# Optimization experiments

Hardware: AMD Instinct MI355X
Metric: run time of the kernel (lower is better)

## Reference

```python
import jax, jax.numpy as jnp
import numpy as np

SCALE = 10.0
KB = 1.0  # kernel_bandwidth

B, D, P, M, K = 128, 128, 4, 100000, 10


def _sqdist(a, b):
    # a: [..., N, D], b: [..., M, D] -> squared euclidean [..., N, M]
    a2 = jnp.sum(a * a, axis=-1)[..., :, None]
    b2 = jnp.sum(b * b, axis=-1)[..., None, :]
    ab = jnp.einsum('...nd,...md->...nm', a, b)
    return jnp.maximum(a2 + b2 - 2.0 * ab, 0.0)


def setup_inputs() -> dict:
    key = jax.random.key(0)
    k1, k2, k3, k4, k5, k6, k7 = jax.random.split(key, 7)
    return {
        'global_img_feat': jax.random.normal(k1, (B, D), jnp.float32),
        'global_text_feat': jax.random.normal(k2, (B, D), jnp.float32),
        'local_img_feats': jax.random.normal(k3, (P, B, D), jnp.float32),
        'centers': jax.random.normal(k4, (P, M, D), jnp.float32),
        'cross_indices': jax.random.randint(k5, (B, K), 0, M, jnp.int64),
        'position': jax.random.randint(k6, (B,), 0, M, jnp.int64),
        'memory_vid': jax.random.randint(k7, (M,), 0, 1000, jnp.int64),
    }


def reference(global_img_feat, global_text_feat, local_img_feats, centers,
              cross_indices, position, memory_vid):
    b = global_img_feat.shape[0]
    # ---- global MMD alignment (text branch detached) ----
    img = global_img_feat / jnp.linalg.norm(global_img_feat, axis=1, keepdims=True)
    txt_d = jax.lax.stop_gradient(global_text_feat)
    txt = txt_d / jnp.linalg.norm(txt_d, axis=1, keepdims=True)
    inv2kb2 = 1.0 / (2.0 * KB * KB)
    k_xx = jnp.exp(-_sqdist(img, img) * inv2kb2)
    k_yy = jnp.exp(-_sqdist(txt, txt) * inv2kb2)
    k_xy = jnp.exp(-_sqdist(img, txt) * inv2kb2)
    off = ~jnp.eye(b, dtype=bool)
    denom = b * (b - 1)
    mmd = (jnp.sum(jnp.where(off, k_xx, 0.0)) / denom
           + jnp.sum(jnp.where(off, k_yy, 0.0)) / denom
           - 2.0 * jnp.mean(k_xy))
    # ---- local part contrastive loss (vectorized over P parts) ----
    m = centers.shape[1]
    pos_feat = centers[:, cross_indices]                       # [P,B,K,D]
    f2 = jnp.sum(local_img_feats ** 2, axis=-1)                # [P,B]
    p2 = jnp.sum(pos_feat ** 2, axis=-1)                       # [P,B,K]
    fp = jnp.einsum('pbd,pbkd->pbk', local_img_feats, pos_feat)
    pos_dist = jnp.sqrt(jnp.maximum(f2[..., None] + p2 - 2.0 * fp, 0.0))  # [P,B,K]
    neg_dist = jnp.sqrt(_sqdist(local_img_feats, centers))     # [P,B,M]
    # negative mask over memory slots (int indices are constants)
    neg_mask = jnp.ones((m,), bool).at[cross_indices.reshape(-1)].set(False)
    neg_mask = neg_mask.at[position].set(False)
    x = jnp.log(jnp.sum(jnp.exp(-SCALE * pos_dist), axis=-1))  # [P,B]
    y = jnp.log(jnp.sum(jnp.exp(-SCALE * neg_dist) * neg_mask[None, None, :], axis=-1))
    l = jnp.sum(-x + y, axis=1) / local_img_feats.shape[1]     # [P]
    l = jnp.where(jnp.isnan(l), 0.0, l)
    local_loss = jnp.sum(l) / local_img_feats.shape[0]
    total = local_loss + 1.0 * mmd
    pos_vid = memory_vid[cross_indices]                        # [B,K]
    return total, local_loss, mmd, pos_vid
```

## Files before the change

kernel.cpp:

```cpp
#include <hip/hip_runtime.h>
#include <math.h>

#define B_ 128
#define D_ 128
#define P_ 4
#define M_ 100000
#define K_ 10
#define SCALE_ 10.0f
#define TPP 1563
#define NEG_BLOCKS 256
#define MMD_BLOCKS 128
#define POS_BLOCKS 128
#define D2_CUT 120.0f

typedef short bf16x8 __attribute__((ext_vector_type(8)));
typedef float floatx4 __attribute__((ext_vector_type(4)));

__device__ inline unsigned pack_bf16_trunc(unsigned f0, unsigned f1) {
    return __builtin_amdgcn_perm(f1, f0, 0x07060302u);
}

template <int CTRL>
__device__ inline float dpp_add(float v) {
    int x = __builtin_amdgcn_update_dpp(0, __builtin_bit_cast(int, v), CTRL, 0xF, 0xF, true);
    return v + __builtin_bit_cast(float, x);
}
__device__ inline float row16Sum(float v) {
    v = dpp_add<0xB1>(v);
    v = dpp_add<0x4E>(v);
    v = dpp_add<0x141>(v);
    v = dpp_add<0x140>(v);
    return v;
}
__device__ inline float waveSum64(float v) {
    v = row16Sum(v);
    v += __shfl_xor(v, 16, 64);
    v += __shfl_xor(v, 32, 64);
    return v;
}
__device__ inline float waveReduceSumOld(float v) {
    #pragma unroll
    for (int off = 32; off > 0; off >>= 1) v += __shfl_xor(v, off, 64);
    return v;
}
__device__ inline float blockReduce128(float v, float* sh2) {
    v = waveSum64(v);
    int wid = threadIdx.x >> 6;
    if ((threadIdx.x & 63) == 0) sh2[wid] = v;
    __syncthreads();
    float r = sh2[0] + sh2[1];
    __syncthreads();
    return r;
}

__global__ __launch_bounds__(128) void k_prep(const float* __restrict__ img,
                                              const float* __restrict__ txt,
                                              const float* __restrict__ local,
                                              float* imgT, float* txtT,
                                              float* a2i, float* a2t,
                                              float* f2w, float* s_neg,
                                              bf16x8* __restrict__ Apk) {
    __shared__ float sh2[2];
    int bid = blockIdx.x, t = threadIdx.x;
    if (bid < 256) {
        int row = bid & 127, which = bid >> 7;
        if (bid < 4) s_neg[bid * 128 + t] = 0.f;
        const float* src = which ? txt : img;
        float* dstT = which ? txtT : imgT;
        float* a2 = which ? a2t : a2i;
        float v = src[row * D_ + t];
        float s = blockReduce128(v * v, sh2);
        float n = v / sqrtf(s);
        dstT[t * 128 + row] = n;
        float s2 = blockReduce128(n * n, sh2);
        if (t == 0) a2[row] = s2;
    } else if (bid < 768) {
        int r = bid - 256;
        float v = local[(size_t)r * D_ + t];
        float s = blockReduce128(v * v, sh2);
        if (t == 0) f2w[r] = s;
    } else {
        int g = (bid - 768) * 128 + t;
        int p = g >> 11, f = g & 2047;
        int fl = f & 63, bt = (f >> 6) & 7, kc = f >> 9;
        int row = bt * 16 + (fl & 15);
        int col = kc * 32 + ((fl >> 4) & 3) * 8;
        const float* lp = local + (size_t)p * B_ * D_ + row * D_ + col;
        const uint4 u0 = *(const uint4*)lp;
        const uint4 u1 = *(const uint4*)(lp + 4);
        union { bf16x8 v; unsigned u[4]; } fr;
        fr.u[0] = pack_bf16_trunc(u0.x, u0.y);
        fr.u[1] = pack_bf16_trunc(u0.z, u0.w);
        fr.u[2] = pack_bf16_trunc(u1.x, u1.y);
        fr.u[3] = pack_bf16_trunc(u1.z, u1.w);
        Apk[g] = fr.v;
    }
}

__global__ __launch_bounds__(256, 2) void k_main(const float* __restrict__ local,
                                                 const float* __restrict__ centers,
                                                 const float* __restrict__ imgT,
                                                 const float* __restrict__ txtT,
                                                 const float* __restrict__ a2i,
                                                 const float* __restrict__ a2t,
                                                 const int* __restrict__ ci,
                                                 const int* __restrict__ posi,
                                                 const int* __restrict__ mvid,
                                                 const float* __restrict__ f2w,
                                                 const bf16x8* __restrict__ Apk,
                                                 float* __restrict__ s_neg,
                                                 float* __restrict__ s_pos,
                                                 double* __restrict__ mmd_part,
                                                 float* __restrict__ out) {
    union Smem {
        struct {
            bf16x8 A_lds[2048];
            float Bt[3][8192];
            float sred[512];
            float f2l[128];
        } n;
        struct {
            float ri[128], rt[128];
            float sh2[2];
        } m;
    };
    __shared__ Smem sm;
    const int bid = blockIdx.x;
    const int t = threadIdx.x;
    const int w = t >> 6;
    const int l = t & 63;

    if (bid < NEG_BLOCKS) {
        const int p = bid >> 6;
        const int g = bid & 63;
        const int nt = (g < 27) ? 25 : 24;
        const int n16 = l & 15;
        const int q = l >> 4;

        if (t < 128) sm.n.f2l[t] = f2w[p * 128 + t];

        const bf16x8* Ap = Apk + (p << 11);
        #pragma unroll
        for (int s8 = 0; s8 < 8; s8++) {
            int fb = w * 64 + 256 * s8;
            __builtin_amdgcn_global_load_lds(
                (const __attribute__((address_space(1))) void*)(Ap + fb + l),
                (__attribute__((address_space(3))) void*)(&sm.n.A_lds[fb]),
                16, 0, 0);
        }

        unsigned soff[8];
        #pragma unroll
        for (int j = 0; j < 8; j++) {
            unsigned d = (unsigned)(w * 8 + j) * 1024u + (unsigned)l * 16u;
            unsigned s = 2u * ((d >> 11) & 3u) + ((d >> 8) & 1u);
            unsigned e = d ^ (s << 4);
            unsigned u = e >> 5, hf = (e >> 4) & 1u;
            soff[j] = (u & 63u) * 512u + (u >> 8) * 128u + ((u >> 6) & 3u) * 32u + hf * 16u;
        }

        const char* cbp = (const char*)(centers + (size_t)p * M_ * D_);
        char* BtBase = (char*)&sm.n.Bt[0][0];

        auto DMA_TILE = [&](int m0, int buf) {
            char* dst = BtBase + buf * 32768 + w * 8192;
            if (m0 + 64 <= M_) {
                const char* srcb = cbp + (size_t)m0 * 512;
                #pragma unroll
                for (int j = 0; j < 8; j++) {
                    __builtin_amdgcn_global_load_lds(
                        (const __attribute__((address_space(1))) void*)(srcb + soff[j]),
                        (__attribute__((address_space(3))) void*)(dst + j * 1024),
                        16, 0, 0);
                }
            } else {
                #pragma unroll
                for (int j = 0; j < 8; j++) {
                    unsigned d = (unsigned)(w * 8 + j) * 1024u + (unsigned)l * 16u;
                    unsigned s = 2u * ((d >> 11) & 3u) + ((d >> 8) & 1u);
                    unsigned e = d ^ (s << 4);
                    unsigned u = e >> 5, hf = (e >> 4) & 1u;
                    int row = m0 + (int)(u & 63u);
                    if (row >= M_) row = M_ - 1;
                    size_t off = (size_t)row * 512 + (u >> 8) * 128 + ((u >> 6) & 3u) * 32 + hf * 16;
                    __builtin_amdgcn_global_load_lds(
                        (const __attribute__((address_space(1))) void*)(cbp + off),
                        (__attribute__((address_space(3))) void*)(dst + j * 1024),
                        16, 0, 0);
                }
            }
        };

        float sacc[8][4];
        #pragma unroll
        for (int bt = 0; bt < 8; bt++)
            #pragma unroll
            for (int r = 0; r < 4; r++) sacc[bt][r] = 0.f;

        int m0 = g * 64;
        DMA_TILE(m0, 0);
        if (nt > 1) DMA_TILE(m0 + 4096, 1);
        int bcur = 0;

        for (int i = 0; i < nt; i++) {
            if (i < nt - 1) asm volatile("s_waitcnt vmcnt(8)" ::: "memory");
            else           asm volatile("s_waitcnt vmcnt(0)" ::: "memory");
            __builtin_amdgcn_s_barrier();

            if (i + 2 < nt) {
                int b2 = bcur + 2; if (b2 >= 3) b2 -= 3;
                DMA_TILE(m0 + 8192, b2);
            }

            const char* bufc = (const char*)(BtBase + bcur * 32768);
            float c2 = 0.f;
            bf16x8 bfr[4];
            #pragma unroll
            for (int kc = 0; kc < 4; kc++) {
                unsigned u = (unsigned)((kc * 4 + q) * 64 + (w * 16 + n16));
                unsigned sb = 2u * (unsigned)q + (unsigned)((n16 >> 3) & 1);
                unsigned a0 = (u * 32u) ^ (sb << 4);
                union { floatx4 f; uint4 ui; } h0, h1;
                h0.f = *(const floatx4*)(bufc + a0);
                h1.f = *(const floatx4*)(bufc + (a0 ^ 16u));
                c2 += h0.f[0]*h0.f[0] + h0.f[1]*h0.f[1] + h0.f[2]*h0.f[2] + h0.f[3]*h0.f[3]
                    + h1.f[0]*h1.f[0] + h1.f[1]*h1.f[1] + h1.f[2]*h1.f[2] + h1.f[3]*h1.f[3];
                union { bf16x8 v; unsigned uu[4]; } fr;
                fr.uu[0] = pack_bf16_trunc(h0.ui.x, h0.ui.y);
                fr.uu[1] = pack_bf16_trunc(h0.ui.z, h0.ui.w);
                fr.uu[2] = pack_bf16_trunc(h1.ui.x, h1.ui.y);
                fr.uu[3] = pack_bf16_trunc(h1.ui.z, h1.ui.w);
                bfr[kc] = fr.v;
            }
            c2 += __shfl_xor(c2, 16, 64);
            c2 += __shfl_xor(c2, 32, 64);
            const float c2v = c2;
            const int gm = m0 + w * 16 + n16;

            floatx4 acc[8];
            #pragma unroll
            for (int bt = 0; bt < 8; bt++) acc[bt] = (floatx4)(0.f);
            #pragma unroll
            for (int kc = 0; kc < 4; kc++) {
                #pragma unroll
                for (int bt = 0; bt < 8; bt++) {
                    bf16x8 af = sm.n.A_lds[kc * 512 + bt * 64 + l];
                    acc[bt] = __builtin_amdgcn_mfma_f32_16x16x32_bf16(af, bfr[kc], acc[bt], 0, 0, 0);
                }
            }

            float dmin = 1e30f;
            #pragma unroll
            for (int bt = 0; bt < 8; bt++) {
                floatx4 f4 = *(const floatx4*)&sm.n.f2l[bt * 16 + q * 4];
                #pragma unroll
                for (int r = 0; r < 4; r++) {
                    float d2 = fmaf(-2.f, acc[bt][r], f4[r] + c2v);
                    dmin = fminf(dmin, d2);
                }
            }
            if (__any(dmin < D2_CUT)) {
                float vm = (gm < M_) ? 1.f : 0.f;
                for (int ii = 0; ii < B_ * K_; ii++) {
                    if (ci[ii] == gm) vm = 0.f;
                }
                for (int ii = 0; ii < B_; ii++) {
                    if (posi[ii] == gm) vm = 0.f;
                }
                #pragma unroll
                for (int bt = 0; bt < 8; bt++) {
                    floatx4 f4 = *(const floatx4*)&sm.n.f2l[bt * 16 + q * 4];
                    #pragma unroll
                    for (int r = 0; r < 4; r++) {
                        float d2 = fmaxf(fmaf(-2.f, acc[bt][r], f4[r] + c2v), 0.f);
                        if (d2 < D2_CUT) sacc[bt][r] += vm * expf(-SCALE_ * sqrtf(d2));
                    }
                }
            }
            m0 += 4096;
            bcur = (bcur + 1 == 3) ? 0 : bcur + 1;
        }

        #pragma unroll
        for (int bt = 0; bt < 8; bt++) {
            #pragma unroll
            for (int r = 0; r < 4; r++) {
                float s = row16Sum(sacc[bt][r]);
                if (n16 == 0) sm.n.sred[w * 128 + bt * 16 + q * 4 + r] = s;
            }
        }
        __syncthreads();
        if (t < 128) {
            float s = sm.n.sred[t] + sm.n.sred[128 + t] + sm.n.sred[256 + t] + sm.n.sred[384 + t];
            if (s != 0.f) atomicAdd(&s_neg[p * 128 + t], s);
        }
    } else if (bid < NEG_BLOCKS + MMD_BLOCKS) {
        const int i = bid - NEG_BLOCKS;
        if (t < 128) {
            sm.m.ri[t] = imgT[t * 128 + i];
            sm.m.rt[t] = txtT[t * 128 + i];
        }
        __syncthreads();
        float kxx = 0.f, kyy = 0.f, kxy = 0.f;
        if (t < 128) {
            float dxx = 0.f, dyy = 0.f, dxy = 0.f;
            #pragma unroll 4
            for (int d = 0; d < D_; d++) {
                float rid = sm.m.ri[d], rtd = sm.m.rt[d];
                float av = imgT[d * 128 + t];
                float bv = txtT[d * 128 + t];
                dxx = fmaf(rid, av, dxx);
                dyy = fmaf(rtd, bv, dyy);
                dxy = fmaf(rid, bv, dxy);
            }
            kxx = (i == t) ? 0.f : expf(-fmaxf(a2i[i] + a2i[t] - 2.f * dxx, 0.f) * 0.5f);
            kyy = (i == t) ? 0.f : expf(-fmaxf(a2t[i] + a2t[t] - 2.f * dyy, 0.f) * 0.5f);
            kxy = expf(-fmaxf(a2i[i] + a2t[t] - 2.f * dxy, 0.f) * 0.5f);
        }
        float sxx = waveReduceSumOld(kxx);
        float syy = waveReduceSumOld(kyy);
        float sxy = waveReduceSumOld(kxy);
        __syncthreads();
        if (t == 0)  { sm.m.sh2[0] = sxx; }
        if (t == 64) { sm.m.sh2[1] = sxx; }
        __syncthreads();
        float txx = sm.m.sh2[0] + sm.m.sh2[1];
        __syncthreads();
        if (t == 0)  { sm.m.sh2[0] = syy; }
        if (t == 64) { sm.m.sh2[1] = syy; }
        __syncthreads();
        float tyy = sm.m.sh2[0] + sm.m.sh2[1];
        __syncthreads();
        if (t == 0)  { sm.m.sh2[0] = sxy; }
        if (t == 64) { sm.m.sh2[1] = sxy; }
        __syncthreads();
        float txy = sm.m.sh2[0] + sm.m.sh2[1];
        if (t == 0) {
            mmd_part[i] = (double)txx;
            mmd_part[128 + i] = (double)tyy;
            mmd_part[256 + i] = (double)txy;
        }
    } else {
        const int pair = (bid - (NEG_BLOCKS + MMD_BLOCKS)) * 4 + w;
        const int p = pair >> 7, b = pair & 127;
        const float* f = local + (size_t)pair * D_;
        float f0 = f[l], f1 = f[l + 64];
        float f2v = f2w[pair];
        const float* cb = centers + (size_t)p * M_ * D_;
        float s = 0.f;
        #pragma unroll
        for (int k = 0; k < K_; k++) {
            int idx = ci[b * K_ + k];
            const float* c = cb + (size_t)idx * D_;
            float c0 = c[l], c1 = c[l + 64];
            float p2 = waveSum64(c0 * c0 + c1 * c1);
            float fp = waveSum64(f0 * c0 + f1 * c1);
            float d2 = fmaxf(f2v + p2 - 2.f * fp, 0.f);
            if (d2 < D2_CUT) s += expf(-SCALE_ * sqrtf(d2));
        }
        if (l == 0) s_pos[pair] = s;
        if (p == 0 && l < K_) {
            int ix = ci[b * K_ + l];
            out[3 + b * K_ + l] = (float)mvid[ix];
        }
    }
}

__global__ __launch_bounds__(512) void k_final(const float* __restrict__ s_pos,
                                               const float* __restrict__ s_neg,
                                               const double* __restrict__ mmd_part,
                                               float* out) {
    __shared__ float red[512];
    __shared__ float lp_[4];
    int t = threadIdx.x;
    float x = logf(s_pos[t]);
    float y = logf(s_neg[t]);
    red[t] = -x + y;
    __syncthreads();
    for (int s = 64; s > 0; s >>= 1) {
        if ((t & 127) < s) red[t] += red[t + s];
        __syncthreads();
    }
    if ((t & 127) == 0) {
        float lv = red[t] / (float)B_;
        if (isnan(lv)) lv = 0.f;
        lp_[t >> 7] = lv;
    }
    __syncthreads();
    if (t == 0) {
        float local_loss = (lp_[0] + lp_[1] + lp_[2] + lp_[3]) / (float)P_;
        double sxx = 0.0, syy = 0.0, sxy = 0.0;
        for (int i = 0; i < 128; i++) {
            sxx += mmd_part[i];
            syy += mmd_part[128 + i];
            sxy += mmd_part[256 + i];
        }
        double denom = 128.0 * 127.0;
        float mmd = (float)(sxx / denom + syy / denom - 2.0 * (sxy / (128.0 * 128.0)));
        out[0] = local_loss + mmd;
        out[1] = local_loss;
        out[2] = mmd;
    }
}

extern "C" void kernel_launch(void* const* d_in, const int* in_sizes, int n_in,
                              void* d_out, int out_size, void* d_ws, size_t ws_size,
                              hipStream_t stream) {
    const float* img     = (const float*)d_in[0];
    const float* txt     = (const float*)d_in[1];
    const float* local   = (const float*)d_in[2];
    const float* centers = (const float*)d_in[3];
    const int*   ci      = (const int*)d_in[4];
    const int*   posi    = (const int*)d_in[5];
    const int*   mvid    = (const int*)d_in[6];
    float* out = (float*)d_out;

    char* ws = (char*)d_ws;
    float*  imgT     = (float*)(ws + 0);
    float*  txtT     = (float*)(ws + 65536);
    float*  a2i      = (float*)(ws + 131072);
    float*  a2t      = (float*)(ws + 131584);
    float*  f2w      = (float*)(ws + 132096);
    float*  s_pos    = (float*)(ws + 134144);
    float*  s_neg    = (float*)(ws + 136192);
    double* mmd_part = (double*)(ws + 138240);
    bf16x8* Apk      = (bf16x8*)(ws + 147456);

    k_prep<<<832, 128, 0, stream>>>(img, txt, local, imgT, txtT, a2i, a2t, f2w, s_neg, Apk);
    k_main<<<NEG_BLOCKS + MMD_BLOCKS + POS_BLOCKS, 256, 0, stream>>>(
        local, centers, imgT, txtT, a2i, a2t, ci, posi, mvid, f2w, Apk,
        s_neg, s_pos, mmd_part, out);
    k_final<<<1, 512, 0, stream>>>(s_pos, s_neg, mmd_part, out);
}
```

Before: 335.7 us.

## Replace LDS triple-buffered DMA with per-wave register double-buffering in separate neg kernel

The negative-distance loop no longer stages center tiles through LDS with block-wide barriers. Each wave now loads its own 16-row tile straight into registers, double-buffered, and works through tiles spaced by a wave stride, with twice as many blocks. The MMD and positive branches move into a separate kernel launched after it. This removes per-tile barriers and LDS traffic, at the cost of more registers, uncoalesced 32-byte row-strided loads, more atomics per block and an extra serialized launch.

After: 344.6 us. 2.6% more time.

```diff
diff --git a/kernel.cpp b/kernel.cpp
--- a/kernel.cpp
+++ b/kernel.cpp
@@ -7,8 +7,9 @@
 #define M_ 100000
 #define K_ 10
 #define SCALE_ 10.0f
-#define TPP 1563
-#define NEG_BLOCKS 256
+#define WPP 512
+#define NT16 6250
+#define NEG_BLOCKS 512
 #define MMD_BLOCKS 128
 #define POS_BLOCKS 128
 #define D2_CUT 120.0f
@@ -97,208 +98,169 @@
     }
 }
 
-__global__ __launch_bounds__(256, 2) void k_main(const float* __restrict__ local,
-                                                 const float* __restrict__ centers,
-                                                 const float* __restrict__ imgT,
-                                                 const float* __restrict__ txtT,
-                                                 const float* __restrict__ a2i,
-                                                 const float* __restrict__ a2t,
-                                                 const int* __restrict__ ci,
-                                                 const int* __restrict__ posi,
-                                                 const int* __restrict__ mvid,
-                                                 const float* __restrict__ f2w,
-                                                 const bf16x8* __restrict__ Apk,
-                                                 float* __restrict__ s_neg,
-                                                 float* __restrict__ s_pos,
-                                                 double* __restrict__ mmd_part,
-                                                 float* __restrict__ out) {
-    union Smem {
-        struct {
-            bf16x8 A_lds[2048];
-            float Bt[3][8192];
-            float sred[512];
-            float f2l[128];
-        } n;
-        struct {
-            float ri[128], rt[128];
-            float sh2[2];
-        } m;
-    };
-    __shared__ Smem sm;
+__device__ __forceinline__ void load_rb(uint4 (&rb)[4][2], const float* cb,
+                                        int tl, int n16, int q) {
+    const uint4* src = (const uint4*)(cb + (size_t)(tl * 16 + n16) * D_ + q * 8);
+    #pragma unroll
+    for (int kc = 0; kc < 4; kc++) {
+        rb[kc][0] = src[kc * 8];
+        rb[kc][1] = src[kc * 8 + 1];
+    }
+}
+
+__device__ __forceinline__ void compute_tile(const uint4 (&rb)[4][2], int tl, bool valid,
+                                             const bf16x8* A_lds, const float* f2l,
+                                             float (&sacc)[8][4],
+                                             const int* __restrict__ ci,
+                                             const int* __restrict__ posi,
+                                             int l, int n16, int q) {
+    float c2 = 0.f;
+    bf16x8 bfr[4];
+    #pragma unroll
+    for (int kc = 0; kc < 4; kc++) {
+        union { uint4 u; floatx4 f; } a, b;
+        a.u = rb[kc][0];
+        b.u = rb[kc][1];
+        c2 += a.f[0]*a.f[0] + a.f[1]*a.f[1] + a.f[2]*a.f[2] + a.f[3]*a.f[3]
+            + b.f[0]*b.f[0] + b.f[1]*b.f[1] + b.f[2]*b.f[2] + b.f[3]*b.f[3];
+        union { bf16x8 v; unsigned u[4]; } fr;
+        fr.u[0] = pack_bf16_trunc(a.u.x, a.u.y);
+        fr.u[1] = pack_bf16_trunc(a.u.z, a.u.w);
+        fr.u[2] = pack_bf16_trunc(b.u.x, b.u.y);
+        fr.u[3] = pack_bf16_trunc(b.u.z, b.u.w);
+        bfr[kc] = fr.v;
+    }
+    c2 += __shfl_xor(c2, 16, 64);
+    c2 += __shfl_xor(c2, 32, 64);
+    const float c2v = c2;
+
+    floatx4 acc[8];
+    #pragma unroll
+    for (int bt = 0; bt < 8; bt++) acc[bt] = (floatx4)(0.f);
+    #pragma unroll
+    for (int kc = 0; kc < 4; kc++) {
+        #pragma unroll
+        for (int bt = 0; bt < 8; bt++) {
+            bf16x8 af = A_lds[kc * 512 + bt * 64 + l];
+            acc[bt] = __builtin_amdgcn_mfma_f32_16x16x32_bf16(af, bfr[kc], acc[bt], 0, 0, 0);
+        }
+    }
+
+    float dmin = 1e30f;
+    #pragma unroll
+    for (int bt = 0; bt < 8; bt++) {
+        floatx4 f4 = *(const floatx4*)&f2l[bt * 16 + q * 4];
+        #pragma unroll
+        for (int r = 0; r < 4; r++) {
+            float d2 = fmaf(-2.f, acc[bt][r], f4[r] + c2v);
+            dmin = fminf(dmin, d2);
+        }
+    }
+    if (valid && __any(dmin < D2_CUT)) {
+        const int gm = tl * 16 + n16;
+        float vm = 1.f;
+        for (int ii = 0; ii < B_ * K_; ii++) {
+            if (ci[ii] == gm) vm = 0.f;
+        }
+        for (int ii = 0; ii < B_; ii++) {
+            if (posi[ii] == gm) vm = 0.f;
+        }
+        #pragma unroll
+        for (int bt = 0; bt < 8; bt++) {
+            floatx4 f4 = *(const floatx4*)&f2l[bt * 16 + q * 4];
+            #pragma unroll
+            for (int r = 0; r < 4; r++) {
+                float d2 = fmaxf(fmaf(-2.f, acc[bt][r], f4[r] + c2v), 0.f);
+                if (d2 < D2_CUT) sacc[bt][r] += vm * expf(-SCALE_ * sqrtf(d2));
+            }
+        }
+    }
+}
+
+__global__ __launch_bounds__(256, 2) void k_neg(const float* __restrict__ centers,
+                                                const int* __restrict__ ci,
+                                                const int* __restrict__ posi,
+                                                const float* __restrict__ f2w,
+                                                const bf16x8* __restrict__ Apk,
+                                                float* __restrict__ s_neg) {
+    __shared__ bf16x8 A_lds[2048];
+    __shared__ float f2l[128];
     const int bid = blockIdx.x;
     const int t = threadIdx.x;
     const int w = t >> 6;
     const int l = t & 63;
-
-    if (bid < NEG_BLOCKS) {
-        const int p = bid >> 6;
-        const int g = bid & 63;
-        const int nt = (g < 27) ? 25 : 24;
-        const int n16 = l & 15;
-        const int q = l >> 4;
-
-        if (t < 128) sm.n.f2l[t] = f2w[p * 128 + t];
-
-        const bf16x8* Ap = Apk + (p << 11);
-        #pragma unroll
-        for (int s8 = 0; s8 < 8; s8++) {
-            int fb = w * 64 + 256 * s8;
-            __builtin_amdgcn_global_load_lds(
-                (const __attribute__((address_space(1))) void*)(Ap + fb + l),
-                (__attribute__((address_space(3))) void*)(&sm.n.A_lds[fb]),
-                16, 0, 0);
-        }
-
-        unsigned soff[8];
-        #pragma unroll
-        for (int j = 0; j < 8; j++) {
-            unsigned d = (unsigned)(w * 8 + j) * 1024u + (unsigned)l * 16u;
-            unsigned s = 2u * ((d >> 11) & 3u) + ((d >> 8) & 1u);
-            unsigned e = d ^ (s << 4);
-            unsigned u = e >> 5, hf = (e >> 4) & 1u;
-            soff[j] = (u & 63u) * 512u + (u >> 8) * 128u + ((u >> 6) & 3u) * 32u + hf * 16u;
-        }
-
-        const char* cbp = (const char*)(centers + (size_t)p * M_ * D_);
-        char* BtBase = (char*)&sm.n.Bt[0][0];
-
-        auto DMA_TILE = [&](int m0, int buf) {
-            char* dst = BtBase + buf * 32768 + w * 8192;
-            if (m0 + 64 <= M_) {
-                const char* srcb = cbp + (size_t)m0 * 512;
-                #pragma unroll
-                for (int j = 0; j < 8; j++) {
-                    __builtin_amdgcn_global_load_lds(
-                        (const __attribute__((address_space(1))) void*)(srcb + soff[j]),
-                        (__attribute__((address_space(3))) void*)(dst + j * 1024),
-                        16, 0, 0);
-                }
-            } else {
-                #pragma unroll
-                for (int j = 0; j < 8; j++) {
-                    unsigned d = (unsigned)(w * 8 + j) * 1024u + (unsigned)l * 16u;
-                    unsigned s = 2u * ((d >> 11) & 3u) + ((d >> 8) & 1u);
-                    unsigned e = d ^ (s << 4);
-                    unsigned u = e >> 5, hf = (e >> 4) & 1u;
-                    int row = m0 + (int)(u & 63u);
-                    if (row >= M_) row = M_ - 1;
-                    size_t off = (size_t)row * 512 + (u >> 8) * 128 + ((u >> 6) & 3u) * 32 + hf * 16;
-                    __builtin_amdgcn_global_load_lds(
-                        (const __attribute__((address_space(1))) void*)(cbp + off),
-                        (__attribute__((address_space(3))) void*)(dst + j * 1024),
-                        16, 0, 0);
-                }
-            }
-        };
-
-        float sacc[8][4];
-        #pragma unroll
-        for (int bt = 0; bt < 8; bt++)
-            #pragma unroll
-            for (int r = 0; r < 4; r++) sacc[bt][r] = 0.f;
-
-        int m0 = g * 64;
-        DMA_TILE(m0, 0);
-        if (nt > 1) DMA_TILE(m0 + 4096, 1);
-        int bcur = 0;
-
-        for (int i = 0; i < nt; i++) {
-            if (i < nt - 1) asm volatile("s_waitcnt vmcnt(8)" ::: "memory");
-            else           asm volatile("s_waitcnt vmcnt(0)" ::: "memory");
-            __builtin_amdgcn_s_barrier();
-
-            if (i + 2 < nt) {
-                int b2 = bcur + 2; if (b2 >= 3) b2 -= 3;
-                DMA_TILE(m0 + 8192, b2);
-            }
-
-            const char* bufc = (const char*)(BtBase + bcur * 32768);
-            float c2 = 0.f;
-            bf16x8 bfr[4];
-            #pragma unroll
-            for (int kc = 0; kc < 4; kc++) {
-                unsigned u = (unsigned)((kc * 4 + q) * 64 + (w * 16 + n16));
-                unsigned sb = 2u * (unsigned)q + (unsigned)((n16 >> 3) & 1);
-                unsigned a0 = (u * 32u) ^ (sb << 4);
-                union { floatx4 f; uint4 ui; } h0, h1;
-                h0.f = *(const floatx4*)(bufc + a0);
-                h1.f = *(const floatx4*)(bufc + (a0 ^ 16u));
-                c2 += h0.f[0]*h0.f[0] + h0.f[1]*h0.f[1] + h0.f[2]*h0.f[2] + h0.f[3]*h0.f[3]
-                    + h1.f[0]*h1.f[0] + h1.f[1]*h1.f[1] + h1.f[2]*h1.f[2] + h1.f[3]*h1.f[3];
-                union { bf16x8 v; unsigned uu[4]; } fr;
-                fr.uu[0] = pack_bf16_trunc(h0.ui.x, h0.ui.y);
-                fr.uu[1] = pack_bf16_trunc(h0.ui.z, h0.ui.w);
-                fr.uu[2] = pack_bf16_trunc(h1.ui.x, h1.ui.y);
-                fr.uu[3] = pack_bf16_trunc(h1.ui.z, h1.ui.w);
-                bfr[kc] = fr.v;
-            }
-            c2 += __shfl_xor(c2, 16, 64);
-            c2 += __shfl_xor(c2, 32, 64);
-            const float c2v = c2;
-            const int gm = m0 + w * 16 + n16;
-
-            floatx4 acc[8];
-            #pragma unroll
-            for (int bt = 0; bt < 8; bt++) acc[bt] = (floatx4)(0.f);
-            #pragma unroll
-            for (int kc = 0; kc < 4; kc++) {
-                #pragma unroll
-                for (int bt = 0; bt < 8; bt++) {
-                    bf16x8 af = sm.n.A_lds[kc * 512 + bt * 64 + l];
-                    acc[bt] = __builtin_amdgcn_mfma_f32_16x16x32_bf16(af, bfr[kc], acc[bt], 0, 0, 0);
-                }
-            }
-
-            float dmin = 1e30f;
-            #pragma unroll
-            for (int bt = 0; bt < 8; bt++) {
-                floatx4 f4 = *(const floatx4*)&sm.n.f2l[bt * 16 + q * 4];
-                #pragma unroll
-                for (int r = 0; r < 4; r++) {
-                    float d2 = fmaf(-2.f, acc[bt][r], f4[r] + c2v);
-                    dmin = fminf(dmin, d2);
-                }
-            }
-            if (__any(dmin < D2_CUT)) {
-                float vm = (gm < M_) ? 1.f : 0.f;
-                for (int ii = 0; ii < B_ * K_; ii++) {
-                    if (ci[ii] == gm) vm = 0.f;
-                }
-                for (int ii = 0; ii < B_; ii++) {
-                    if (posi[ii] == gm) vm = 0.f;
-                }
-                #pragma unroll
-                for (int bt = 0; bt < 8; bt++) {
-                    floatx4 f4 = *(const floatx4*)&sm.n.f2l[bt * 16 + q * 4];
-                    #pragma unroll
-                    for (int r = 0; r < 4; r++) {
-                        float d2 = fmaxf(fmaf(-2.f, acc[bt][r], f4[r] + c2v), 0.f);
-                        if (d2 < D2_CUT) sacc[bt][r] += vm * expf(-SCALE_ * sqrtf(d2));
-                    }
-                }
-            }
-            m0 += 4096;
-            bcur = (bcur + 1 == 3) ? 0 : bcur + 1;
-        }
-
-        #pragma unroll
-        for (int bt = 0; bt < 8; bt++) {
-            #pragma unroll
-            for (int r = 0; r < 4; r++) {
-                float s = row16Sum(sacc[bt][r]);
-                if (n16 == 0) sm.n.sred[w * 128 + bt * 16 + q * 4 + r] = s;
-            }
-        }
-        __syncthreads();
+    const int p = bid >> 7;
+    const int v = ((bid & 127) << 2) + w;
+    const int n16 = l & 15;
+    const int q = l >> 4;
+
+    const bf16x8* Ap = Apk + (p << 11);
+    #pragma unroll
+    for (int s8 = 0; s8 < 8; s8++) {
+        int fb = w * 64 + 256 * s8;
+        __builtin_amdgcn_global_load_lds(
+            (const __attribute__((address_space(1))) void*)(Ap + fb + l),
+            (__attribute__((address_space(3))) void*)(&A_lds[fb]),
+            16, 0, 0);
+    }
+    if (t < 128) f2l[t] = f2w[p * 128 + t];
+    __syncthreads();
+
+    const float* cb = centers + (size_t)p * M_ * D_;
+
+    float sacc[8][4];
+    #pragma unroll
+    for (int bt = 0; bt < 8; bt++)
+        #pragma unroll
+        for (int r = 0; r < 4; r++) sacc[bt][r] = 0.f;
+
+    uint4 rbA[4][2], rbB[4][2];
+    load_rb(rbA, cb, v, n16, q);
+    for (int jj = 0; jj < 6; jj++) {
+        const int t1 = v + (2 * jj + 1) * WPP;
+        load_rb(rbB, cb, t1, n16, q);
+        compute_tile(rbA, v + 2 * jj * WPP, true, A_lds, f2l, sacc, ci, posi, l, n16, q);
+        const int t2i = v + (2 * jj + 2) * WPP;
+        load_rb(rbA, cb, (t2i < NT16) ? t2i : 0, n16, q);
+        compute_tile(rbB, t1, true, A_lds, f2l, sacc, ci, posi, l, n16, q);
+    }
+    const int t12 = v + 12 * WPP;
+    compute_tile(rbA, t12, t12 < NT16, A_lds, f2l, sacc, ci, posi, l, n16, q);
+
+    #pragma unroll
+    for (int bt = 0; bt < 8; bt++) {
+        #pragma unroll
+        for (int r = 0; r < 4; r++) {
+            float s = row16Sum(sacc[bt][r]);
+            if (n16 == 0 && s != 0.f)
+                atomicAdd(&s_neg[p * 128 + bt * 16 + q * 4 + r], s);
+        }
+    }
+}
+
+__global__ __launch_bounds__(256) void k_mp(const float* __restrict__ local,
+                                            const float* __restrict__ centers,
+                                            const float* __restrict__ imgT,
+                                            const float* __restrict__ txtT,
+                                            const float* __restrict__ a2i,
+                                            const float* __restrict__ a2t,
+                                            const int* __restrict__ ci,
+                                            const int* __restrict__ mvid,
+                                            const float* __restrict__ f2w,
+                                            float* __restrict__ s_pos,
+                                            double* __restrict__ mmd_part,
+                                            float* __restrict__ out) {
+    __shared__ float ri[128], rt[128], sh2[2];
+    const int bid = blockIdx.x;
+    const int t = threadIdx.x;
+    const int w = t >> 6;
+    const int l = t & 63;
+
+    if (bid < MMD_BLOCKS) {
+        const int i = bid;
         if (t < 128) {
-            float s = sm.n.sred[t] + sm.n.sred[128 + t] + sm.n.sred[256 + t] + sm.n.sred[384 + t];
-            if (s != 0.f) atomicAdd(&s_neg[p * 128 + t], s);
-        }
-    } else if (bid < NEG_BLOCKS + MMD_BLOCKS) {
-        const int i = bid - NEG_BLOCKS;
-        if (t < 128) {
-            sm.m.ri[t] = imgT[t * 128 + i];
-            sm.m.rt[t] = txtT[t * 128 + i];
+            ri[t] = imgT[t * 128 + i];
+            rt[t] = txtT[t * 128 + i];
         }
         __syncthreads();
         float kxx = 0.f, kyy = 0.f, kxy = 0.f;
@@ -306,7 +268,7 @@
             float dxx = 0.f, dyy = 0.f, dxy = 0.f;
             #pragma unroll 4
             for (int d = 0; d < D_; d++) {
-                float rid = sm.m.ri[d], rtd = sm.m.rt[d];
+                float rid = ri[d], rtd = rt[d];
                 float av = imgT[d * 128 + t];
                 float bv = txtT[d * 128 + t];
                 dxx = fmaf(rid, av, dxx);
@@ -321,27 +283,27 @@
         float syy = waveReduceSumOld(kyy);
         float sxy = waveReduceSumOld(kxy);
         __syncthreads();
-        if (t == 0)  { sm.m.sh2[0] = sxx; }
-        if (t == 64) { sm.m.sh2[1] = sxx; }
-        __syncthreads();
-        float txx = sm.m.sh2[0] + sm.m.sh2[1];
-        __syncthreads();
-        if (t == 0)  { sm.m.sh2[0] = syy; }
-        if (t == 64) { sm.m.sh2[1] = syy; }
-        __syncthreads();
-        float tyy = sm.m.sh2[0] + sm.m.sh2[1];
-        __syncthreads();
-        if (t == 0)  { sm.m.sh2[0] = sxy; }
-        if (t == 64) { sm.m.sh2[1] = sxy; }
-        __syncthreads();
-        float txy = sm.m.sh2[0] + sm.m.sh2[1];
+        if (t == 0)  { sh2[0] = sxx; }
+        if (t == 64) { sh2[1] = sxx; }
+        __syncthreads();
+        float txx = sh2[0] + sh2[1];
+        __syncthreads();
+        if (t == 0)  { sh2[0] = syy; }
+        if (t == 64) { sh2[1] = syy; }
+        __syncthreads();
+        float tyy = sh2[0] + sh2[1];
+        __syncthreads();
+        if (t == 0)  { sh2[0] = sxy; }
+        if (t == 64) { sh2[1] = sxy; }
+        __syncthreads();
+        float txy = sh2[0] + sh2[1];
         if (t == 0) {
             mmd_part[i] = (double)txx;
             mmd_part[128 + i] = (double)tyy;
             mmd_part[256 + i] = (double)txy;
         }
     } else {
-        const int pair = (bid - (NEG_BLOCKS + MMD_BLOCKS)) * 4 + w;
+        const int pair = (bid - MMD_BLOCKS) * 4 + w;
         const int p = pair >> 7, b = pair & 127;
         const float* f = local + (size_t)pair * D_;
         float f0 = f[l], f1 = f[l + 64];
@@ -427,8 +389,8 @@
     bf16x8* Apk      = (bf16x8*)(ws + 147456);
 
     k_prep<<<832, 128, 0, stream>>>(img, txt, local, imgT, txtT, a2i, a2t, f2w, s_neg, Apk);
-    k_main<<<NEG_BLOCKS + MMD_BLOCKS + POS_BLOCKS, 256, 0, stream>>>(
-        local, centers, imgT, txtT, a2i, a2t, ci, posi, mvid, f2w, Apk,
-        s_neg, s_pos, mmd_part, out);
+    k_neg<<<NEG_BLOCKS, 256, 0, stream>>>(centers, ci, posi, f2w, Apk, s_neg);
+    k_mp<<<MMD_BLOCKS + POS_BLOCKS, 256, 0, stream>>>(
+        local, centers, imgT, txtT, a2i, a2t, ci, mvid, f2w, s_pos, mmd_part, out);
     k_final<<<1, 512, 0, stream>>>(s_pos, s_neg, mmd_part, out);
 }
```
